# Performance work log

Measured on AMD Instinct MI355X. Metric: run time of the kernel, lower is better.

## Reference

```python
import jax, jax.numpy as jnp
import numpy as np
import math

NUM_ITER = 5
FEAT_STRIDE = 16
GAUSS_SIGMA = 1.0
HINGE_THRESHOLD = -999.0
MIN_FILTER_REG = 1e-3
ALPHA_EPS = 0.0


def apply_filter(feat, weights):
    # feat: (ni, ns, C, H, W); weights: (ns, C, fH, fW) -> scores (ni, ns, oH, oW)
    ni, ns, C, H, W = feat.shape
    fH, fW = weights.shape[-2], weights.shape[-1]
    x = feat.reshape(ni, ns * C, H, W)
    out = jax.lax.conv_general_dilated(
        x, weights, window_strides=(1, 1),
        padding=((fH // 2, fH // 2), (fW // 2, fW // 2)),
        dimension_numbers=('NCHW', 'OIHW', 'NCHW'),
        feature_group_count=ns)
    return out  # (ni, ns, oH, oW); oH = H + (fH+1)%2


def get_label(center, out_sz, sigma):
    # center: (ni, ns, 2) in (row, col) order
    k0 = jnp.arange(out_sz[0], dtype=jnp.float32)[None, None, :, None]
    k1 = jnp.arange(out_sz[1], dtype=jnp.float32)[None, None, None, :]
    g0 = jnp.exp(-0.5 / (sigma * sigma) * (k0 - center[..., 0][..., None, None]) ** 2)
    g1 = jnp.exp(-0.5 / (sigma * sigma) * (k1 - center[..., 1][..., None, None]) ** 2)
    return g0 * g1  # (ni, ns, oH, oW)


def _forward(weights, feat, bb, log_step_length, filter_reg):
    ni, ns = feat.shape[0], feat.shape[1]
    fH, fW = weights.shape[-2], weights.shape[-1]
    out_sz = (feat.shape[-2] + (fH + 1) % 2, feat.shape[-1] + (fW + 1) % 2)
    step = jnp.exp(log_step_length)[0]
    reg = jnp.maximum(filter_reg * filter_reg, MIN_FILTER_REG ** 2)[0]
    dmap_offset = jnp.array([fH % 2, fW % 2], jnp.float32) / 2.0
    # (x, y) -> (row, col), feature-grid coordinates
    center = ((bb[..., :2] + bb[..., 2:] / 2.0) / FEAT_STRIDE)[..., ::-1] - dmap_offset
    label = get_label(center, out_sz, GAUSS_SIGMA)
    mask = (label > HINGE_THRESHOLD).astype(feat.dtype)
    label = label * mask
    sw = math.sqrt(1.0 / ni)

    losses = []
    for _ in range(NUM_ITER):
        scores = apply_filter(feat, weights)
        scores_act = mask * scores + (1.0 - mask) * jax.nn.relu(scores)
        score_mask = mask + (1.0 - mask) * (jax.lax.stop_gradient(scores) > 0).astype(scores.dtype)
        residuals = sw * (scores_act - label)
        losses.append((jnp.sum(residuals ** 2) + reg * jnp.sum(weights ** 2)) / ns)
        residuals_mapped = score_mask * (sw * residuals)
        # feat-transpose = adjoint of apply_filter w.r.t. the filter weights
        _, vjp_fn = jax.vjp(lambda w: apply_filter(feat, w), weights)
        data_grad = vjp_fn(residuals_mapped)[0]
        weights_grad = data_grad + reg * weights
        scores_grad = apply_filter(feat, weights_grad)
        scores_grad = sw * (score_mask * scores_grad)
        alpha_num = jnp.sum(weights_grad ** 2, axis=(1, 2, 3))  # (ns,)
        alpha_den = jnp.maximum(
            jnp.sum(scores_grad.reshape(ni, ns, -1) ** 2, axis=(0, 2))
            + (reg + ALPHA_EPS) * alpha_num, 1e-8)
        alpha = alpha_num / alpha_den
        weights = weights - step * alpha[:, None, None, None] * weights_grad

    scores = apply_filter(feat, weights)
    scores = mask * scores + (1.0 - mask) * jax.nn.relu(scores)
    losses.append((jnp.sum((sw * (scores - label)) ** 2) + reg * jnp.sum(weights ** 2)) / ns)
    return weights, jnp.stack(losses)


def setup_inputs() -> dict:
    key = jax.random.key(0)
    k1, k2, k3, k4 = jax.random.split(key, 4)
    ni, ns, C, H, W, fH, fW = 3, 32, 512, 22, 22, 4, 4
    weights = 0.01 * jax.random.normal(k1, (ns, C, fH, fW), jnp.float32)
    feat = jax.random.normal(k2, (ni, ns, C, H, W), jnp.float32)
    # boxes (x, y, w, h) in image coords (image size = 22*16 = 352)
    xy = jax.random.uniform(k3, (ni, ns, 2), jnp.float32, 50.0, 250.0)
    wh = jax.random.uniform(k4, (ni, ns, 2), jnp.float32, 32.0, 96.0)
    bb = jnp.concatenate([xy, wh], axis=-1)
    log_step_length = jnp.zeros((1,), jnp.float32)  # log(1.0)
    filter_reg = 0.01 * jnp.ones((1,), jnp.float32)
    return {"weights": weights, "feat": feat, "bb": bb,
            "log_step_length": log_step_length, "filter_reg": filter_reg}


def reference(weights, feat, bb, log_step_length, filter_reg):
    return _forward(weights, feat, bb, log_step_length, filter_reg)
```

## Files before the change

kernel.cpp:

```cpp
#include <hip/hip_runtime.h>
#include <hip/hip_fp16.h>

#define NI 3
#define NS 32
#define CHN 512
#define OH 23
#define P2 529
#define NP 50784
#define UV 484
#define WSZ 262144

typedef unsigned int uint32;
typedef unsigned short u16;
typedef _Float16 h2 __attribute__((ext_vector_type(2)));
typedef _Float16 f16x8 __attribute__((ext_vector_type(8)));
typedef float f32x4 __attribute__((ext_vector_type(4)));

#define OFF_FEATT 0UL
#define OFF_LABEL 47579136UL
#define OFF_S0    47782272UL
#define OFF_S1    47985408UL
#define OFF_SGRAW 48188544UL
#define OFF_WG    48391680UL
#define OFF_WGF16 49440256UL
#define OFF_W0F16 49964544UL
#define OFF_PART  50488832UL

#define P_DEN   0
#define P_NUM   4320
#define P_LOSS  5600
#define P_WSQ0  5760
#define P_WSQA  5792
#define P_WSQ5  6816
#define P_L5    7840

__device__ __forceinline__ float waveSum(float v) {
#pragma unroll
  for (int o = 32; o > 0; o >>= 1) v += __shfl_xor(v, o, 64);
  return v;
}

__device__ __forceinline__ float alphaFor(const float* __restrict__ part, int t, int s,
                                          float reg) {
  const float* np_ = part + P_NUM + (size_t)(t * NS + s) * 8;
  const float* dp_ = part + P_DEN + (size_t)(t * NS + s) * 3;
  float nu = 0.f;
#pragma unroll
  for (int i = 0; i < 8; ++i) nu += np_[i];
  float de = dp_[0] + dp_[1] + dp_[2];
  return nu / fmaxf(de + reg * nu, 1e-8f);
}

__global__ __launch_bounds__(256) void k_setup(const float* __restrict__ feat,
                                               const float* __restrict__ w0,
                                               const float* __restrict__ bb,
                                               u16* __restrict__ featT,
                                               u16* __restrict__ w0f16,
                                               float* __restrict__ wmaster,
                                               float* __restrict__ label,
                                               float* __restrict__ part) {
  __shared__ float ldsT[7744];
  __shared__ float sred[4];
  int b = blockIdx.x, tid = threadIdx.x;
  if (b < 3072) {
    int snT = b >> 5, r5 = b & 31;
    int cb = r5 >> 2, uvq = r5 & 3;
    int s = snT / 3, n = snT % 3;
    const float* fsrc =
        feat + ((size_t)n * NS + s) * CHN * UV + (size_t)(cb * 64) * UV + uvq * 121;
#pragma unroll
    for (int it = 0; it < 31; ++it) {
      int idx = it * 256 + tid;
      if (idx < 7744) {
        int r = (unsigned)idx / 121u;
        int j = idx - r * 121;
        ldsT[idx] = fsrc[r * 484 + j];
      }
    }
    __syncthreads();
    uint32* dstb = (uint32*)featT +
                   ((size_t)(snT * 4 + (cb >> 1)) * UV + uvq * 121) * 64 + (cb & 1) * 32;
#pragma unroll
    for (int it = 0; it < 16; ++it) {
      int o = it * 256 + tid;
      if (o < 3872) {
        int uv = o >> 5, k = o & 31;
        float f0 = ldsT[(2 * k) * 121 + uv];
        float f1 = ldsT[(2 * k + 1) * 121 + uv];
        uint32 pk = (uint32)__half_as_ushort(__float2half(f0)) |
                    ((uint32)__half_as_ushort(__float2half(f1)) << 16);
        dstb[(size_t)uv * 64 + k] = pk;
      }
    }
  } else if (b < 3104) {
    int s = b - 3072;
    for (int i = tid; i < 8192; i += 256) {
      int tap = i >> 9, c = i & 511;
      w0f16[(size_t)s * 8192 + i] =
          __half_as_ushort(__float2half(w0[(size_t)s * 8192 + c * 16 + tap]));
    }
    float sq = 0.f;
    for (int i = tid; i < 8192; i += 256) {
      float v = w0[(size_t)s * 8192 + i];
      wmaster[(size_t)s * 8192 + i] = v;
      sq += v * v;
    }
    sq = waveSum(sq);
    if ((tid & 63) == 0) sred[tid >> 6] = sq;
    __syncthreads();
    if (tid == 0) part[P_WSQ0 + s] = sred[0] + sred[1] + sred[2] + sred[3];
  } else {
    int p = (b - 3104) * 256 + tid;
    if (p < NP) {
      int nsid = p / P2, rem = p % P2;
      int i = rem / OH, j = rem % OH;
      const float* bp = bb + (size_t)nsid * 4;
      float cr = (bp[1] + 0.5f * bp[3]) * 0.0625f;
      float cc = (bp[0] + 0.5f * bp[2]) * 0.0625f;
      float dy = (float)i - cr, dx = (float)j - cc;
      label[p] = __expf(-0.5f * (dy * dy + dx * dx));
    }
  }
}

__global__ __launch_bounds__(1024) void k_conv_fwd(const u16* __restrict__ featT,
                                                   const u16* __restrict__ wf16,
                                                   float* __restrict__ outbuf, int t,
                                                   float* __restrict__ part) {
  __shared__ uint32 w_lds[16 * 260];
  __shared__ float G[496 * 17];
  __shared__ float dred[16];
  int tid = threadIdx.x;
  int snT = blockIdx.x;
  int s = snT / 3, n = snT - s * 3;
  const uint32* wsrc = (const uint32*)(wf16 + (size_t)s * 8192);
  for (int i = tid; i < 4096; i += 1024) {
    int tap = i >> 8, p = i & 255;
    w_lds[tap * 260 + p] = wsrc[i];
  }
  __syncthreads();
  int wave = tid >> 6, lane = tid & 63;
  int q = lane >> 4, m16 = lane & 15;
  int t0 = wave, t1 = (wave < 15) ? wave + 16 : wave;
  f32x4 acc0 = {0.f, 0.f, 0.f, 0.f}, acc1 = {0.f, 0.f, 0.f, 0.f};
  size_t base = (size_t)snT * 4 * UV * 128;
  size_t row0 = (size_t)(t0 * 16 + m16) * 128;
  size_t row1 = (size_t)(t1 * 16 + m16) * 128;
#pragma unroll
  for (int step = 0; step < 16; ++step) {
    int cb = step >> 2, cin = (step & 3) * 32;
    size_t cbase = base + (size_t)cb * UV * 128 + cin + q * 8;
    f16x8 a0 = *(const f16x8*)(featT + cbase + row0);
    f16x8 a1 = *(const f16x8*)(featT + cbase + row1);
    uint4 bw = *(const uint4*)&w_lds[m16 * 260 + step * 16 + q * 4];
    f16x8 bf = __builtin_bit_cast(f16x8, bw);
    acc0 = __builtin_amdgcn_mfma_f32_16x16x32_f16(a0, bf, acc0, 0, 0, 0);
    acc1 = __builtin_amdgcn_mfma_f32_16x16x32_f16(a1, bf, acc1, 0, 0, 0);
  }
#pragma unroll
  for (int r = 0; r < 4; ++r) G[(t0 * 16 + q * 4 + r) * 17 + m16] = acc0[r];
  if (wave < 15) {
#pragma unroll
    for (int r = 0; r < 4; ++r) G[(t1 * 16 + q * 4 + r) * 17 + m16] = acc1[r];
  }
  __syncthreads();
  float dsq = 0.f;
  int p = tid;
  if (p < P2) {
    int y = p / 23, x = p - y * 23;
    float val = 0.f;
#pragma unroll
    for (int ky = 0; ky < 4; ++ky) {
      int u = y + ky - 2;
      if ((unsigned)u < 22u) {
#pragma unroll
        for (int kx = 0; kx < 4; ++kx) {
          int v = x + kx - 2;
          if ((unsigned)v < 22u) val += G[(u * 22 + v) * 17 + ky * 4 + kx];
        }
      }
    }
    outbuf[(size_t)(n * NS + s) * P2 + p] = val;
    dsq = val * val;
  }
  if (t >= 0) {
    dsq = waveSum(dsq);
    if (lane == 0) dred[wave] = dsq;
    __syncthreads();
    if (tid == 0) {
      float dsum = 0.f;
#pragma unroll
      for (int i = 0; i < 16; ++i) dsum += dred[i];
      part[P_DEN + (size_t)(t * NS + s) * 3 + n] = dsum * (1.0f / 3.0f);
    }
  }
}

__global__ __launch_bounds__(768) void k_adjoint(
    int t, const u16* __restrict__ featT, const float* __restrict__ label,
    const float* __restrict__ scores_old, float* __restrict__ scores_new,
    const float* __restrict__ sgraw, float* __restrict__ wg, u16* __restrict__ wgf16,
    float* __restrict__ wmaster, float* __restrict__ part, const float* __restrict__ lsl,
    const float* __restrict__ fr) {
  __shared__ float r_lds[1950];
  __shared__ float red[12288];
  __shared__ float lred[12];
  __shared__ float nred2[2], wred2[2];
  int tid = threadIdx.x;
  int s = blockIdx.x >> 3, chunk = blockIdx.x & 7;
  int c0 = chunk * 64;
  int cp = tid & 31, tg1 = (tid >> 5) & 1, m = tid >> 6;
  int n = m >> 2, uq = m & 3;
  int u0 = (uq * 22) >> 2, u1 = ((uq + 1) * 22) >> 2;
  float step = __expf(lsl[0]);
  float frv = fr[0];
  float reg = fmaxf(frv * frv, 1e-6f);
  float alpha_p = (t >= 1) ? alphaFor(part, t - 1, s, reg) : 0.f;
  for (int i = tid; i < 1950; i += 768) r_lds[i] = 0.f;
  __syncthreads();
  float lsum = 0.f;
  for (int pl = tid; pl < 1587; pl += 768) {
    int nn = pl / P2, rem = pl % P2;
    int y = rem / OH, x = rem % OH;
    size_t gp = (size_t)(nn * NS + s) * P2 + rem;
    float S = scores_old[gp];
    if (t >= 1) S -= step * alpha_p * sgraw[gp];
    float d = S - label[gp];
    r_lds[nn * 650 + (y + 1) * 26 + (x + 1)] = d * (1.0f / 3.0f);
    if (chunk == 0) {
      if (t >= 1) scores_new[gp] = S;
      lsum += d * d;
    }
  }
  lsum = waveSum(lsum);
  if ((tid & 63) == 0) lred[tid >> 6] = lsum;
  __syncthreads();
  if (chunk == 0 && tid == 0) {
    float L = 0.f;
#pragma unroll
    for (int i = 0; i < 12; ++i) L += lred[i];
    part[P_LOSS + t * NS + s] = L * (1.0f / 3.0f);
  }
  const uint32* fb = (const uint32*)featT +
                     ((size_t)(s * 3 + n) * 4 + (chunk >> 1)) * UV * 64 +
                     (chunk & 1) * 32 + cp;
  float ac[16];
#pragma unroll
  for (int i = 0; i < 16; ++i) ac[i] = 0.f;
  const float* rbase = r_lds + n * 650;
  for (int u = u0; u < u1; ++u) {
    const float* rA = rbase + (u + 3 - tg1) * 26;
    const float* rB = rbase + (u + 1 - tg1) * 26;
    const uint32* fp_ = fb + (size_t)u * 22 * 64;
#pragma unroll
    for (int v = 0; v < 22; ++v) {
      uint32 fv = fp_[(size_t)v * 64];
      h2 hv = __builtin_bit_cast(h2, fv);
      float f0 = (float)hv[0], f1 = (float)hv[1];
#pragma unroll
      for (int kx = 0; kx < 4; ++kx) {
        float ra = rA[v + 3 - kx];
        float rb_ = rB[v + 3 - kx];
        ac[0 + kx] = fmaf(f0, ra, ac[0 + kx]);
        ac[4 + kx] = fmaf(f0, rb_, ac[4 + kx]);
        ac[8 + kx] = fmaf(f1, ra, ac[8 + kx]);
        ac[12 + kx] = fmaf(f1, rb_, ac[12 + kx]);
      }
    }
  }
#pragma unroll
  for (int cj = 0; cj < 2; ++cj)
#pragma unroll
    for (int kyi = 0; kyi < 2; ++kyi)
#pragma unroll
      for (int kx = 0; kx < 4; ++kx) {
        int ky = tg1 + 2 * kyi;
        int j = (cj * 4 + ky) * 4 + kx;
        red[(j * 12 + m) * 32 + cp] = ac[cj * 8 + kyi * 4 + kx];
      }
  __syncthreads();
  if (tid < 128) {
    int ocp = tid & 31, ky = tid >> 5;
    float wsq_part = 0.f, num_part = 0.f;
#pragma unroll
    for (int jj = 0; jj < 8; ++jj) {
      int cj = jj >> 2, kx = jj & 3;
      int j = (cj * 4 + ky) * 4 + kx;
      float dg = 0.f;
#pragma unroll
      for (int mm = 0; mm < 12; ++mm) dg += red[(j * 12 + mm) * 32 + ocp];
      int c = c0 + 2 * ocp + cj;
      int tap = ky * 4 + kx;
      size_t widx = (size_t)s * 8192 + (size_t)c * 16 + tap;
      float wold = wmaster[widx];
      float wnew = wold;
      if (t >= 1) {
        wnew = wold - step * alpha_p * wg[widx];
        wmaster[widx] = wnew;
      }
      float wgn = dg + reg * wnew;
      wg[widx] = wgn;
      wgf16[(size_t)s * 8192 + tap * 512 + c] = __half_as_ushort(__float2half(wgn));
      wsq_part += wnew * wnew;
      num_part += wgn * wgn;
    }
    wsq_part = waveSum(wsq_part);
    num_part = waveSum(num_part);
    if ((tid & 63) == 0) {
      nred2[tid >> 6] = num_part;
      wred2[tid >> 6] = wsq_part;
    }
  }
  __syncthreads();
  if (tid == 0) {
    part[P_NUM + (size_t)(t * NS + s) * 8 + chunk] = nred2[0] + nred2[1];
    if (t >= 1) part[P_WSQA + (size_t)((t - 1) * NS + s) * 8 + chunk] = wred2[0] + wred2[1];
  }
}

__global__ void k_final(float* __restrict__ wmaster, const float* __restrict__ wg,
                        const float* __restrict__ scores4, const float* __restrict__ sgraw,
                        const float* __restrict__ label, float* __restrict__ part,
                        const float* __restrict__ lsl, const float* __restrict__ fr) {
  __shared__ float alpha_s[32];
  __shared__ float red4[4];
  int b = blockIdx.x, tid = threadIdx.x;
  float step = __expf(lsl[0]);
  float frv = fr[0];
  float reg = fmaxf(frv * frv, 1e-6f);
  if (tid < 32) alpha_s[tid] = alphaFor(part, 4, tid, reg);
  __syncthreads();
  if (b < 1024) {
    int idx = b * 256 + tid;
    int s = idx >> 13;
    float w5 = wmaster[idx] - step * alpha_s[s] * wg[idx];
    wmaster[idx] = w5;
    float sq = waveSum(w5 * w5);
    if ((tid & 63) == 0) red4[tid >> 6] = sq;
    __syncthreads();
    if (tid == 0) part[P_WSQ5 + b] = red4[0] + red4[1] + red4[2] + red4[3];
  } else {
    int p = (b - 1024) * 256 + tid;
    float contrib = 0.f;
    if (p < NP) {
      int nsid = p / P2;
      int s = nsid & 31;
      float s5 = scores4[p] - step * alpha_s[s] * sgraw[p];
      float d = s5 - label[p];
      contrib = d * d;
    }
    contrib = waveSum(contrib);
    if ((tid & 63) == 0) red4[tid >> 6] = contrib;
    __syncthreads();
    if (tid == 0)
      part[P_L5 + (b - 1024)] = (red4[0] + red4[1] + red4[2] + red4[3]) * (1.0f / 3.0f);
  }
}

__global__ void k_losses(float* __restrict__ out_losses, const float* __restrict__ part,
                         const float* __restrict__ fr) {
  __shared__ float red[8];
  int tid = threadIdx.x;
  float frv = fr[0];
  float reg = fmaxf(frv * frv, 1e-6f);
  float v5 = 0.f;
  for (int i = tid; i < 1024; i += 256) v5 += part[P_WSQ5 + i];
  v5 = waveSum(v5);
  if ((tid & 63) == 0) red[tid >> 6] = v5;
  __syncthreads();
  float wsq5 = red[0] + red[1] + red[2] + red[3];
  float l5 = 0.f;
  for (int i = tid; i < 199; i += 256) l5 += part[P_L5 + i];
  l5 = waveSum(l5);
  if ((tid & 63) == 0) red[4 + (tid >> 6)] = l5;
  __syncthreads();
  float loss5 = red[4] + red[5] + red[6] + red[7];
  if (tid < 5) {
    int t = tid;
    float ls = 0.f;
    for (int i = 0; i < 32; ++i) ls += part[P_LOSS + t * NS + i];
    float ws_ = 0.f;
    if (t == 0) {
      for (int i = 0; i < 32; ++i) ws_ += part[P_WSQ0 + i];
    } else {
      for (int i = 0; i < 256; ++i) ws_ += part[P_WSQA + (t - 1) * 256 + i];
    }
    out_losses[t] = (ls + reg * ws_) * (1.0f / 32.0f);
  }
  if (tid == 5) out_losses[5] = (loss5 + reg * wsq5) * (1.0f / 32.0f);
}

extern "C" void kernel_launch(void* const* d_in, const int* in_sizes, int n_in,
                              void* d_out, int out_size, void* d_ws, size_t ws_size,
                              hipStream_t stream) {
  const float* w0 = (const float*)d_in[0];
  const float* feat = (const float*)d_in[1];
  const float* bb = (const float*)d_in[2];
  const float* lsl = (const float*)d_in[3];
  const float* fr = (const float*)d_in[4];
  float* out = (float*)d_out;
  char* ws = (char*)d_ws;
  u16* featT = (u16*)(ws + OFF_FEATT);
  float* label = (float*)(ws + OFF_LABEL);
  float* s0 = (float*)(ws + OFF_S0);
  float* s1 = (float*)(ws + OFF_S1);
  float* sgraw = (float*)(ws + OFF_SGRAW);
  float* wg = (float*)(ws + OFF_WG);
  u16* wgf16 = (u16*)(ws + OFF_WGF16);
  u16* w0f16 = (u16*)(ws + OFF_W0F16);
  float* part = (float*)(ws + OFF_PART);

  k_setup<<<3303, 256, 0, stream>>>(feat, w0, bb, featT, w0f16, out, label, part);
  k_conv_fwd<<<96, 1024, 0, stream>>>(featT, w0f16, s0, -1, part);
  float* sbuf[2] = {s0, s1};
  for (int t = 0; t < 5; ++t) {
    const float* so = (t == 0) ? s0 : sbuf[(t - 1) & 1];
    float* sn = sbuf[t & 1];
    k_adjoint<<<256, 768, 0, stream>>>(t, featT, label, so, sn, sgraw, wg, wgf16, out, part,
                                       lsl, fr);
    k_conv_fwd<<<96, 1024, 0, stream>>>(featT, wgf16, sgraw, t, part);
  }
  k_final<<<1223, 256, 0, stream>>>(out, wg, s0, sgraw, label, part, lsl, fr);
  k_losses<<<1, 256, 0, stream>>>(out + WSZ, part, fr);
}
```

Measured before the change: 397.7 us.

## Recast adjoint filter gradient as MFMA GEMM over channel-major fp16 features

```diff
diff --git a/kernel.cpp b/kernel.cpp
--- a/kernel.cpp
+++ b/kernel.cpp
@@ -12,7 +12,6 @@
 
 typedef unsigned int uint32;
 typedef unsigned short u16;
-typedef _Float16 h2 __attribute__((ext_vector_type(2)));
 typedef _Float16 f16x8 __attribute__((ext_vector_type(8)));
 typedef float f32x4 __attribute__((ext_vector_type(4)));
 
@@ -25,14 +24,18 @@
 #define OFF_WGF16 49440256UL
 #define OFF_W0F16 49964544UL
 #define OFF_PART  50488832UL
+#define OFF_FEATC 50505216UL
+#define OFF_DG    100836864UL
 
 #define P_DEN   0
-#define P_NUM   4320
-#define P_LOSS  5600
-#define P_WSQ0  5760
-#define P_WSQA  5792
-#define P_WSQ5  6816
-#define P_L5    7840
+#define P_NUM   480
+#define P_LOSS  640
+#define P_WSQ0  1120
+#define P_WSQA  1152
+#define P_WSQ5  1280
+#define P_L5    2304
+
+#define APITCH 536
 
 __device__ __forceinline__ float waveSum(float v) {
 #pragma unroll
@@ -42,11 +45,8 @@
 
 __device__ __forceinline__ float alphaFor(const float* __restrict__ part, int t, int s,
                                           float reg) {
-  const float* np_ = part + P_NUM + (size_t)(t * NS + s) * 8;
+  float nu = part[P_NUM + t * NS + s];
   const float* dp_ = part + P_DEN + (size_t)(t * NS + s) * 3;
-  float nu = 0.f;
-#pragma unroll
-  for (int i = 0; i < 8; ++i) nu += np_[i];
   float de = dp_[0] + dp_[1] + dp_[2];
   return nu / fmaxf(de + reg * nu, 1e-8f);
 }
@@ -55,6 +55,7 @@
                                                const float* __restrict__ w0,
                                                const float* __restrict__ bb,
                                                u16* __restrict__ featT,
+                                               u16* __restrict__ featC,
                                                u16* __restrict__ w0f16,
                                                float* __restrict__ wmaster,
                                                float* __restrict__ label,
@@ -90,6 +91,22 @@
         uint32 pk = (uint32)__half_as_ushort(__float2half(f0)) |
                     ((uint32)__half_as_ushort(__float2half(f1)) << 16);
         dstb[(size_t)uv * 64 + k] = pk;
+      }
+    }
+    u16* cdst = featC + ((size_t)snT * 512 + cb * 64) * 512 + uvq * 121;
+#pragma unroll
+    for (int it = 0; it < 31; ++it) {
+      int idx = it * 256 + tid;
+      if (idx < 7744) {
+        int r = (unsigned)idx / 121u;
+        int j = idx - r * 121;
+        cdst[(size_t)r * 512 + j] = __half_as_ushort(__float2half(ldsT[r * 121 + j]));
+      }
+    }
+    if (uvq == 3) {
+      for (int i = tid; i < 64 * 28; i += 256) {
+        int r = i / 28, j = i - r * 28;
+        cdst[(size_t)r * 512 + 121 + 28 + j] = 0;
       }
     }
   } else if (b < 3104) {
@@ -123,6 +140,15 @@
   }
 }
 
+__global__ __launch_bounds__(256) void k_padzero(u16* __restrict__ featC) {
+  int snT = blockIdx.x, tid = threadIdx.x;
+  u16* base = featC + (size_t)snT * 512 * 512;
+  for (int i = tid; i < 512 * 28; i += 256) {
+    int c = i / 28, j = i - c * 28;
+    base[(size_t)c * 512 + 484 + j] = 0;
+  }
+}
+
 __global__ __launch_bounds__(1024) void k_conv_fwd(const u16* __restrict__ featT,
                                                    const u16* __restrict__ wf16,
                                                    float* __restrict__ outbuf, int t,
@@ -196,125 +222,120 @@
   }
 }
 
-__global__ __launch_bounds__(768) void k_adjoint(
-    int t, const u16* __restrict__ featT, const float* __restrict__ label,
+__global__ __launch_bounds__(1024) void k_adjoint_gemm(
+    int t, const u16* __restrict__ featC, const float* __restrict__ label,
     const float* __restrict__ scores_old, float* __restrict__ scores_new,
-    const float* __restrict__ sgraw, float* __restrict__ wg, u16* __restrict__ wgf16,
-    float* __restrict__ wmaster, float* __restrict__ part, const float* __restrict__ lsl,
+    const float* __restrict__ sgraw, float* __restrict__ dgpart,
+    float* __restrict__ part, const float* __restrict__ lsl,
     const float* __restrict__ fr) {
-  __shared__ float r_lds[1950];
-  __shared__ float red[12288];
-  __shared__ float lred[12];
-  __shared__ float nred2[2], wred2[2];
+  __shared__ float d_arr[529];
+  __shared__ _Float16 A_lds[16 * APITCH];
+  __shared__ float lred[16];
   int tid = threadIdx.x;
-  int s = blockIdx.x >> 3, chunk = blockIdx.x & 7;
-  int c0 = chunk * 64;
-  int cp = tid & 31, tg1 = (tid >> 5) & 1, m = tid >> 6;
-  int n = m >> 2, uq = m & 3;
-  int u0 = (uq * 22) >> 2, u1 = ((uq + 1) * 22) >> 2;
+  int snT = blockIdx.x;
+  int s = snT / 3, n = snT - s * 3;
   float step = __expf(lsl[0]);
   float frv = fr[0];
   float reg = fmaxf(frv * frv, 1e-6f);
   float alpha_p = (t >= 1) ? alphaFor(part, t - 1, s, reg) : 0.f;
-  for (int i = tid; i < 1950; i += 768) r_lds[i] = 0.f;
-  __syncthreads();
+  for (int i = tid; i < 16 * APITCH / 2; i += 1024) ((uint32*)A_lds)[i] = 0u;
   float lsum = 0.f;
-  for (int pl = tid; pl < 1587; pl += 768) {
-    int nn = pl / P2, rem = pl % P2;
-    int y = rem / OH, x = rem % OH;
-    size_t gp = (size_t)(nn * NS + s) * P2 + rem;
+  if (tid < P2) {
+    size_t gp = (size_t)(n * NS + s) * P2 + tid;
     float S = scores_old[gp];
-    if (t >= 1) S -= step * alpha_p * sgraw[gp];
+    if (t >= 1) {
+      S -= step * alpha_p * sgraw[gp];
+      scores_new[gp] = S;
+    }
     float d = S - label[gp];
-    r_lds[nn * 650 + (y + 1) * 26 + (x + 1)] = d * (1.0f / 3.0f);
-    if (chunk == 0) {
-      if (t >= 1) scores_new[gp] = S;
-      lsum += d * d;
-    }
+    d_arr[tid] = d;
+    lsum = d * d;
   }
   lsum = waveSum(lsum);
   if ((tid & 63) == 0) lred[tid >> 6] = lsum;
   __syncthreads();
-  if (chunk == 0 && tid == 0) {
+  if (tid == 0) {
     float L = 0.f;
 #pragma unroll
-    for (int i = 0; i < 12; ++i) L += lred[i];
-    part[P_LOSS + t * NS + s] = L * (1.0f / 3.0f);
-  }
-  const uint32* fb = (const uint32*)featT +
-                     ((size_t)(s * 3 + n) * 4 + (chunk >> 1)) * UV * 64 +
-                     (chunk & 1) * 32 + cp;
-  float ac[16];
-#pragma unroll
-  for (int i = 0; i < 16; ++i) ac[i] = 0.f;
-  const float* rbase = r_lds + n * 650;
-  for (int u = u0; u < u1; ++u) {
-    const float* rA = rbase + (u + 3 - tg1) * 26;
-    const float* rB = rbase + (u + 1 - tg1) * 26;
-    const uint32* fp_ = fb + (size_t)u * 22 * 64;
-#pragma unroll
-    for (int v = 0; v < 22; ++v) {
-      uint32 fv = fp_[(size_t)v * 64];
-      h2 hv = __builtin_bit_cast(h2, fv);
-      float f0 = (float)hv[0], f1 = (float)hv[1];
-#pragma unroll
-      for (int kx = 0; kx < 4; ++kx) {
-        float ra = rA[v + 3 - kx];
-        float rb_ = rB[v + 3 - kx];
-        ac[0 + kx] = fmaf(f0, ra, ac[0 + kx]);
-        ac[4 + kx] = fmaf(f0, rb_, ac[4 + kx]);
-        ac[8 + kx] = fmaf(f1, ra, ac[8 + kx]);
-        ac[12 + kx] = fmaf(f1, rb_, ac[12 + kx]);
-      }
-    }
-  }
-#pragma unroll
-  for (int cj = 0; cj < 2; ++cj)
-#pragma unroll
-    for (int kyi = 0; kyi < 2; ++kyi)
-#pragma unroll
-      for (int kx = 0; kx < 4; ++kx) {
-        int ky = tg1 + 2 * kyi;
-        int j = (cj * 4 + ky) * 4 + kx;
-        red[(j * 12 + m) * 32 + cp] = ac[cj * 8 + kyi * 4 + kx];
-      }
-  __syncthreads();
-  if (tid < 128) {
-    int ocp = tid & 31, ky = tid >> 5;
-    float wsq_part = 0.f, num_part = 0.f;
-#pragma unroll
-    for (int jj = 0; jj < 8; ++jj) {
-      int cj = jj >> 2, kx = jj & 3;
-      int j = (cj * 4 + ky) * 4 + kx;
-      float dg = 0.f;
-#pragma unroll
-      for (int mm = 0; mm < 12; ++mm) dg += red[(j * 12 + mm) * 32 + ocp];
-      int c = c0 + 2 * ocp + cj;
-      int tap = ky * 4 + kx;
-      size_t widx = (size_t)s * 8192 + (size_t)c * 16 + tap;
-      float wold = wmaster[widx];
-      float wnew = wold;
-      if (t >= 1) {
-        wnew = wold - step * alpha_p * wg[widx];
-        wmaster[widx] = wnew;
-      }
-      float wgn = dg + reg * wnew;
-      wg[widx] = wgn;
-      wgf16[(size_t)s * 8192 + tap * 512 + c] = __half_as_ushort(__float2half(wgn));
-      wsq_part += wnew * wnew;
-      num_part += wgn * wgn;
-    }
-    wsq_part = waveSum(wsq_part);
-    num_part = waveSum(num_part);
-    if ((tid & 63) == 0) {
-      nred2[tid >> 6] = num_part;
-      wred2[tid >> 6] = wsq_part;
-    }
+    for (int i = 0; i < 16; ++i) L += lred[i];
+    part[P_LOSS + (size_t)(t * NS + s) * 3 + n] = L * (1.0f / 3.0f);
+  }
+  for (int idx = tid; idx < 7744; idx += 1024) {
+    int tap = (unsigned)idx / 484u;
+    int k = idx - tap * 484;
+    int u = (unsigned)k / 22u, v = k - u * 22;
+    int y = u + 2 - (tap >> 2), x = v + 2 - (tap & 3);
+    if ((unsigned)y < 23u && (unsigned)x < 23u)
+      A_lds[tap * APITCH + k] = (_Float16)(d_arr[y * 23 + x] * (1.0f / 3.0f));
+  }
+  __syncthreads();
+  int wave = tid >> 6, lane = tid & 63;
+  int q = lane >> 4, m16 = lane & 15;
+  int ct0 = wave * 2, ct1 = wave * 2 + 1;
+  f32x4 acc0 = {0.f, 0.f, 0.f, 0.f}, acc1 = {0.f, 0.f, 0.f, 0.f};
+  const _Float16* arow = A_lds + m16 * APITCH + q * 8;
+  const u16* b0r = featC + ((size_t)snT * 512 + ct0 * 16 + m16) * 512 + q * 8;
+  const u16* b1r = featC + ((size_t)snT * 512 + ct1 * 16 + m16) * 512 + q * 8;
+#pragma unroll
+  for (int step = 0; step < 16; ++step) {
+    f16x8 a = *(const f16x8*)(arow + step * 32);
+    f16x8 b0 = *(const f16x8*)(b0r + step * 32);
+    f16x8 b1 = *(const f16x8*)(b1r + step * 32);
+    acc0 = __builtin_amdgcn_mfma_f32_16x16x32_f16(a, b0, acc0, 0, 0, 0);
+    acc1 = __builtin_amdgcn_mfma_f32_16x16x32_f16(a, b1, acc1, 0, 0, 0);
+  }
+  float* dgb = dgpart + (size_t)snT * 8192;
+#pragma unroll
+  for (int r = 0; r < 4; ++r) {
+    int tap = q * 4 + r;
+    dgb[tap * 512 + ct0 * 16 + m16] = acc0[r];
+    dgb[tap * 512 + ct1 * 16 + m16] = acc1[r];
+  }
+}
+
+__global__ __launch_bounds__(256) void k_wupd(int t, const float* __restrict__ dgpart,
+                                              float* __restrict__ wmaster,
+                                              float* __restrict__ wg,
+                                              u16* __restrict__ wgf16,
+                                              float* __restrict__ part,
+                                              const float* __restrict__ lsl,
+                                              const float* __restrict__ fr) {
+  __shared__ float nred[4], wred[4];
+  int s = blockIdx.x, tid = threadIdx.x;
+  float step = __expf(lsl[0]);
+  float frv = fr[0];
+  float reg = fmaxf(frv * frv, 1e-6f);
+  float alpha_p = (t >= 1) ? alphaFor(part, t - 1, s, reg) : 0.f;
+  const float* d0 = dgpart + (size_t)(s * 3 + 0) * 8192;
+  const float* d1 = dgpart + (size_t)(s * 3 + 1) * 8192;
+  const float* d2 = dgpart + (size_t)(s * 3 + 2) * 8192;
+  float num = 0.f, wsq = 0.f;
+  for (int j = tid; j < 8192; j += 256) {
+    int tap = j >> 9, c = j & 511;
+    float dg = d0[j] + d1[j] + d2[j];
+    size_t widx = (size_t)s * 8192 + (size_t)c * 16 + tap;
+    float wold = wmaster[widx];
+    float wnew = wold;
+    if (t >= 1) {
+      wnew = wold - step * alpha_p * wg[widx];
+      wmaster[widx] = wnew;
+    }
+    float wgn = dg + reg * wnew;
+    wg[widx] = wgn;
+    wgf16[(size_t)s * 8192 + j] = __half_as_ushort(__float2half(wgn));
+    wsq += wnew * wnew;
+    num += wgn * wgn;
+  }
+  num = waveSum(num);
+  wsq = waveSum(wsq);
+  if ((tid & 63) == 0) {
+    nred[tid >> 6] = num;
+    wred[tid >> 6] = wsq;
   }
   __syncthreads();
   if (tid == 0) {
-    part[P_NUM + (size_t)(t * NS + s) * 8 + chunk] = nred2[0] + nred2[1];
-    if (t >= 1) part[P_WSQA + (size_t)((t - 1) * NS + s) * 8 + chunk] = wred2[0] + wred2[1];
+    part[P_NUM + t * NS + s] = nred[0] + nred[1] + nred[2] + nred[3];
+    if (t >= 1) part[P_WSQA + (t - 1) * NS + s] = wred[0] + wred[1] + wred[2] + wred[3];
   }
 }
 
@@ -378,12 +399,12 @@
   if (tid < 5) {
     int t = tid;
     float ls = 0.f;
-    for (int i = 0; i < 32; ++i) ls += part[P_LOSS + t * NS + i];
+    for (int i = 0; i < 96; ++i) ls += part[P_LOSS + t * 96 + i];
     float ws_ = 0.f;
     if (t == 0) {
       for (int i = 0; i < 32; ++i) ws_ += part[P_WSQ0 + i];
     } else {
-      for (int i = 0; i < 256; ++i) ws_ += part[P_WSQA + (t - 1) * 256 + i];
+      for (int i = 0; i < 32; ++i) ws_ += part[P_WSQA + (t - 1) * 32 + i];
     }
     out_losses[t] = (ls + reg * ws_) * (1.0f / 32.0f);
   }
@@ -401,6 +422,7 @@
   float* out = (float*)d_out;
   char* ws = (char*)d_ws;
   u16* featT = (u16*)(ws + OFF_FEATT);
+  u16* featC = (u16*)(ws + OFF_FEATC);
   float* label = (float*)(ws + OFF_LABEL);
   float* s0 = (float*)(ws + OFF_S0);
   float* s1 = (float*)(ws + OFF_S1);
@@ -408,16 +430,19 @@
   float* wg = (float*)(ws + OFF_WG);
   u16* wgf16 = (u16*)(ws + OFF_WGF16);
   u16* w0f16 = (u16*)(ws + OFF_W0F16);
+  float* dgpart = (float*)(ws + OFF_DG);
   float* part = (float*)(ws + OFF_PART);
 
-  k_setup<<<3303, 256, 0, stream>>>(feat, w0, bb, featT, w0f16, out, label, part);
+  k_setup<<<3303, 256, 0, stream>>>(feat, w0, bb, featT, featC, w0f16, out, label, part);
+  k_padzero<<<96, 256, 0, stream>>>(featC);
   k_conv_fwd<<<96, 1024, 0, stream>>>(featT, w0f16, s0, -1, part);
   float* sbuf[2] = {s0, s1};
   for (int t = 0; t < 5; ++t) {
     const float* so = (t == 0) ? s0 : sbuf[(t - 1) & 1];
     float* sn = sbuf[t & 1];
-    k_adjoint<<<256, 768, 0, stream>>>(t, featT, label, so, sn, sgraw, wg, wgf16, out, part,
-                                       lsl, fr);
+    k_adjoint_gemm<<<96, 1024, 0, stream>>>(t, featC, label, so, sn, sgraw, dgpart, part,
+                                            lsl, fr);
+    k_wupd<<<32, 256, 0, stream>>>(t, dgpart, out, wg, wgf16, part, lsl, fr);
     k_conv_fwd<<<96, 1024, 0, stream>>>(featT, wgf16, sgraw, t, part);
   }
   k_final<<<1223, 256, 0, stream>>>(out, wg, s0, sgraw, label, part, lsl, fr);
```

Measured after the change: 517.4 us. 30.1% more time.
